# Kernel optimization log

Measured on AMD Instinct MI355X. Metric: run time of the kernel, lower is better.

Reference implementation:

```python
import jax, jax.numpy as jnp
import numpy as np

FACTOR = 5


def setup_inputs() -> dict:
    key = jax.random.key(0)
    k1, k2, k3 = jax.random.split(key, 3)
    B, L, H, E = 8, 3072, 8, 64
    return {
        "queries": jax.random.normal(k1, (B, L, H, E), dtype=jnp.float32),
        "keys": jax.random.normal(k2, (B, L, H, E), dtype=jnp.float32),
        "values": jax.random.normal(k3, (B, L, H, E), dtype=jnp.float32),
        "attn_mask": jnp.zeros((1,), dtype=jnp.int32),  # unused, matches torch signature
    }


def _autocorrelation(queries, keys, values):
    B, L, H, E = queries.shape
    # L == S here, so keys/values are used as-is (torch path: values[:, :L])
    qp = jnp.transpose(queries, (0, 2, 3, 1))  # [B,H,E,L]
    kp = jnp.transpose(keys, (0, 2, 3, 1))     # [B,H,E,L]
    vp = jnp.transpose(values, (0, 2, 3, 1))   # [B,H,D,L]

    # period-based dependencies via FFT cross-correlation
    q_fft = jnp.fft.rfft(qp, axis=-1)
    k_fft = jnp.fft.rfft(kp, axis=-1)
    corr = jnp.fft.irfft(q_fft * jnp.conj(k_fft), n=L, axis=-1)  # [B,H,E,L]

    # time-delay aggregation (training branch of the torch module)
    top_k = int(FACTOR * np.log(L))  # static (L known at trace time)
    mean_value = corr.mean(axis=1).mean(axis=1)            # [B,L]
    weights, index = jax.lax.top_k(mean_value, top_k)      # [B,K]
    tmp_corr = jax.nn.softmax(weights, axis=-1)            # [B,K]

    # torch uses only batch-0 shifts: roll(v, -index[0,i]) == gather (t + s) mod L
    shifts = index[0]                                      # [K]
    gather_idx = (jnp.arange(L)[None, :] + shifts[:, None]) % L  # [K,L]

    def step(acc, lag):
        idx_k, w_k = lag                    # idx_k: [L], w_k: [B]
        pattern = vp[..., idx_k]            # [B,H,D,L] rolled gather
        return acc + pattern * w_k[:, None, None, None], None

    agg, _ = jax.lax.scan(step, jnp.zeros_like(vp), (gather_idx, tmp_corr.T))
    return jnp.transpose(agg, (0, 3, 1, 2))  # [B,L,H,D]


def reference(queries, keys, values, attn_mask):
    return _autocorrelation(queries, keys, values)
```

## Files before the change

kernel.cpp:

```cpp
#include <hip/hip_runtime.h>
#include <math.h>

#define L_LEN  3072
#define CH512  512
#define TOPK   40
#define NBATCH 8
#define TWSZ   1088
#define SW(i)  ((i) + ((i) >> 5))
#define FFTSZ  3168
#define SW2(i) ((i) + ((i) >> 4))
#define FFTSZ2 3264

typedef __attribute__((ext_vector_type(2))) float f32x2;

__device__ __forceinline__ void fft3072(float* re, float* im,
                                        const float* Ctab, const float* Stab,
                                        int tid, float sgn)
{
    #pragma unroll
    for (int s = 0; s < 10; s += 2) {
        int q = 1 << s;
        #pragma unroll
        for (int ii = 0; ii < 3; ii++) {
            int ib  = tid + (ii << 8);
            int sub = ib >> 8;
            int t   = ib & 255;
            int pos = t & (q - 1);
            int base= t >> s;
            int i0  = (sub << 10) + (base << (s + 2)) + pos;
            int p0 = SW(i0), p1 = SW(i0 + q), p2 = SW(i0 + 2*q), p3 = SW(i0 + 3*q);
            int j2 = 3 * (pos << (8 - s));
            int ph = j2 + (j2 >> 4);
            float c2 = Ctab[ph], s2 = sgn * Stab[ph];
            float c1 = c2*c2 - s2*s2, s1 = 2.0f*c2*s2;
            float a0r = re[p0], a0i = im[p0];
            float a1r = re[p1], a1i = im[p1];
            float a2r = re[p2], a2i = im[p2];
            float a3r = re[p3], a3i = im[p3];
            float t1r = c1*a1r - s1*a1i, t1i = c1*a1i + s1*a1r;
            float u0r = a0r + t1r, u0i = a0i + t1i;
            float u1r = a0r - t1r, u1i = a0i - t1i;
            float t3r = c1*a3r - s1*a3i, t3i = c1*a3i + s1*a3r;
            float u2r = a2r + t3r, u2i = a2i + t3i;
            float u3r = a2r - t3r, u3i = a2i - t3i;
            float w2r = c2*u2r - s2*u2i, w2i = c2*u2i + s2*u2r;
            float w3r = c2*u3r - s2*u3i, w3i = c2*u3i + s2*u3r;
            float iw3r = -sgn * w3i, iw3i = sgn * w3r;
            re[p0] = u0r + w2r;  im[p0] = u0i + w2i;
            re[p2] = u0r - w2r;  im[p2] = u0i - w2i;
            re[p1] = u1r + iw3r; im[p1] = u1i + iw3i;
            re[p3] = u1r - iw3r; im[p3] = u1i - iw3i;
        }
        __syncthreads();
    }
    #pragma unroll
    for (int ii = 0; ii < 4; ii++) {
        int kk = tid + (ii << 8);
        int ph = kk + (kk >> 4);
        float c1 = Ctab[ph];
        float s1 = sgn * Stab[ph];
        float c2 = c1*c1 - s1*s1;
        float s2 = 2.0f*c1*s1;
        int pk0 = SW(kk), pk1 = SW(1024 + kk), pk2 = SW(2048 + kk);
        float y0r = re[pk0], y0i = im[pk0];
        float y1r = re[pk1], y1i = im[pk1];
        float y2r = re[pk2], y2i = im[pk2];
        float t1r = c1*y1r - s1*y1i, t1i = c1*y1i + s1*y1r;
        float t2r = c2*y2r - s2*y2i, t2i = c2*y2i + s2*y2r;
        float ur = t1r + t2r, ui = t1i + t2i;
        float vr = t1r - t2r, vi = t1i - t2i;
        float mr = y0r - 0.5f*ur, mi = y0i - 0.5f*ui;
        float s3 = sgn * 0.86602540378443864676f;
        re[pk0] = y0r + ur;      im[pk0] = y0i + ui;
        re[pk1] = mr - s3*vi;    im[pk1] = mi + s3*vr;
        re[pk2] = mr + s3*vi;    im[pk2] = mi - s3*vr;
    }
    __syncthreads();
}

__device__ __forceinline__ void fft3072p(f32x2* re, f32x2* im,
                                         const float* Ctab, const float* Stab,
                                         int tid, float sgn)
{
    #pragma unroll
    for (int s = 0; s < 10; s += 2) {
        int q = 1 << s;
        #pragma unroll
        for (int ii = 0; ii < 3; ii++) {
            int ib  = tid + (ii << 8);
            int sub = ib >> 8;
            int t   = ib & 255;
            int pos = t & (q - 1);
            int base= t >> s;
            int i0  = (sub << 10) + (base << (s + 2)) + pos;
            int p0 = SW2(i0), p1 = SW2(i0 + q), p2 = SW2(i0 + 2*q), p3 = SW2(i0 + 3*q);
            int j2 = 3 * (pos << (8 - s));
            int ph = j2 + (j2 >> 4);
            float c2 = Ctab[ph], s2 = sgn * Stab[ph];
            float c1 = c2*c2 - s2*s2, s1 = 2.0f*c2*s2;
            f32x2 a0r = re[p0], a0i = im[p0];
            f32x2 a1r = re[p1], a1i = im[p1];
            f32x2 a2r = re[p2], a2i = im[p2];
            f32x2 a3r = re[p3], a3i = im[p3];
            f32x2 t1r = c1*a1r - s1*a1i, t1i = c1*a1i + s1*a1r;
            f32x2 u0r = a0r + t1r, u0i = a0i + t1i;
            f32x2 u1r = a0r - t1r, u1i = a0i - t1i;
            f32x2 t3r = c1*a3r - s1*a3i, t3i = c1*a3i + s1*a3r;
            f32x2 u2r = a2r + t3r, u2i = a2i + t3i;
            f32x2 u3r = a2r - t3r, u3i = a2i - t3i;
            f32x2 w2r = c2*u2r - s2*u2i, w2i = c2*u2i + s2*u2r;
            f32x2 w3r = c2*u3r - s2*u3i, w3i = c2*u3i + s2*u3r;
            f32x2 iw3r = (-sgn) * w3i, iw3i = sgn * w3r;
            re[p0] = u0r + w2r;  im[p0] = u0i + w2i;
            re[p2] = u0r - w2r;  im[p2] = u0i - w2i;
            re[p1] = u1r + iw3r; im[p1] = u1i + iw3i;
            re[p3] = u1r - iw3r; im[p3] = u1i - iw3i;
        }
        __syncthreads();
    }
    #pragma unroll
    for (int ii = 0; ii < 4; ii++) {
        int kk = tid + (ii << 8);
        int ph = kk + (kk >> 4);
        float c1 = Ctab[ph];
        float s1 = sgn * Stab[ph];
        float c2 = c1*c1 - s1*s1;
        float s2 = 2.0f*c1*s1;
        int pk0 = SW2(kk), pk1 = SW2(1024 + kk), pk2 = SW2(2048 + kk);
        f32x2 y0r = re[pk0], y0i = im[pk0];
        f32x2 y1r = re[pk1], y1i = im[pk1];
        f32x2 y2r = re[pk2], y2i = im[pk2];
        f32x2 t1r = c1*y1r - s1*y1i, t1i = c1*y1i + s1*y1r;
        f32x2 t2r = c2*y2r - s2*y2i, t2i = c2*y2i + s2*y2r;
        f32x2 ur = t1r + t2r, ui = t1i + t2i;
        f32x2 vr = t1r - t2r, vi = t1i - t2i;
        f32x2 mr = y0r - 0.5f*ur, mi = y0i - 0.5f*ui;
        float s3 = sgn * 0.86602540378443864676f;
        re[pk0] = y0r + ur;      im[pk0] = y0i + ui;
        re[pk1] = mr - s3*vi;    im[pk1] = mi + s3*vr;
        re[pk2] = mr + s3*vi;    im[pk2] = mi - s3*vr;
    }
    __syncthreads();
}

__device__ __forceinline__ void fill_twiddles(float* Ctab, float* Stab, int tid)
{
    const float TWO_PI = 6.28318530717958647692f;
    for (int j = tid; j < 1024; j += 256) {
        float ang = TWO_PI * (float)j / 3072.0f;
        float c, s;
        __sincosf(ang, &s, &c);
        int ph = j + (j >> 4);
        Ctab[ph] = c; Stab[ph] = s;
    }
}

__global__ __launch_bounds__(256) void transpose_kernel(
    const float* __restrict__ q, const float* __restrict__ k,
    float* __restrict__ qT, float* __restrict__ kT)
{
    __shared__ float tile[64][65];
    int which = blockIdx.z & 1;
    int b     = blockIdx.z >> 1;
    int l0    = blockIdx.x << 6;
    int c0    = blockIdx.y << 6;
    int x4 = threadIdx.x & 15;
    int y  = threadIdx.x >> 4;
    const float* src = which ? k : q;
    float* dst       = which ? kT : qT;
    size_t in_base = (size_t)b * L_LEN * CH512;
    #pragma unroll
    for (int p = 0; p < 4; p++) {
        int r = y + (p << 4);
        float4 v = *(const float4*)(src + in_base + (size_t)(l0 + r) * CH512 + c0 + (x4 << 2));
        tile[r][(x4 << 2) + 0] = v.x;
        tile[r][(x4 << 2) + 1] = v.y;
        tile[r][(x4 << 2) + 2] = v.z;
        tile[r][(x4 << 2) + 3] = v.w;
    }
    __syncthreads();
    size_t out_base = (size_t)b * CH512 * L_LEN;
    #pragma unroll
    for (int p = 0; p < 4; p++) {
        int c = y + (p << 4);
        float4 w;
        w.x = tile[(x4 << 2) + 0][c];
        w.y = tile[(x4 << 2) + 1][c];
        w.z = tile[(x4 << 2) + 2][c];
        w.w = tile[(x4 << 2) + 3][c];
        *(float4*)(dst + out_base + (size_t)(c0 + c) * L_LEN + l0 + (x4 << 2)) = w;
    }
}

__global__ __launch_bounds__(256, 2) void corr_fft_kernel(
    const float* __restrict__ qT, const float* __restrict__ kT,
    float* __restrict__ S_re, float* __restrict__ S_im)
{
    __shared__ f32x2 re2[FFTSZ2], im2[FFTSZ2];
    __shared__ float Ctab[TWSZ], Stab[TWSZ];
    int blk = blockIdx.x;
    int b   = blk >> 7;
    int c0  = (blk & 127) << 2;
    int tid = threadIdx.x;

    fill_twiddles(Ctab, Stab, tid);

    float accR[12], accI[12];
    #pragma unroll
    for (int it = 0; it < 12; it++) { accR[it] = 0.0f; accI[it] = 0.0f; }

    for (int pp = 0; pp < 2; pp++) {
        int ca = c0 + (pp << 1);
        const float4* qa4 = (const float4*)(qT + ((size_t)b * CH512 + ca) * L_LEN);
        const float4* qb4 = (const float4*)(qT + ((size_t)b * CH512 + ca + 1) * L_LEN);
        const float4* ka4 = (const float4*)(kT + ((size_t)b * CH512 + ca) * L_LEN);
        const float4* kb4 = (const float4*)(kT + ((size_t)b * CH512 + ca + 1) * L_LEN);
        __syncthreads();
        #pragma unroll
        for (int it = 0; it < 3; it++) {
            int idx = tid + (it << 8);
            float4 xqa = qa4[idx], xqb = qb4[idx];
            float4 xka = ka4[idx], xkb = kb4[idx];
            #pragma unroll
            for (int j = 0; j < 4; j++) {
                int n = (idx << 2) + j;
                int m = n / 3;
                int r = n - 3 * m;
                int dst = SW2((r << 10) + (__brev((unsigned)m) >> 22));
                float qav = (j == 0) ? xqa.x : (j == 1) ? xqa.y : (j == 2) ? xqa.z : xqa.w;
                float qbv = (j == 0) ? xqb.x : (j == 1) ? xqb.y : (j == 2) ? xqb.z : xqb.w;
                float kav = (j == 0) ? xka.x : (j == 1) ? xka.y : (j == 2) ? xka.z : xka.w;
                float kbv = (j == 0) ? xkb.x : (j == 1) ? xkb.y : (j == 2) ? xkb.z : xkb.w;
                f32x2 vr = {qav, qbv};
                f32x2 vi = {kav, kbv};
                re2[dst] = vr;
                im2[dst] = vi;
            }
        }
        __syncthreads();
        fft3072p(re2, im2, Ctab, Stab, tid, -1.0f);
        #pragma unroll
        for (int it = 0; it < 12; it++) {
            int f = tid + (it << 8);
            int g = (f == 0) ? 0 : (L_LEN - f);
            int pf = SW2(f), pg = SW2(g);
            f32x2 ar = re2[pf], ai = im2[pf];
            f32x2 br = re2[pg], bi = -im2[pg];
            f32x2 ur = ar + br, ui = ai + bi;
            f32x2 vr = ar - br, vi = ai - bi;
            f32x2 pr = 0.25f * (ur * vi - ui * vr);
            f32x2 pi = 0.25f * (ur * vr + ui * vi);
            accR[it] += pr[0] + pr[1];
            accI[it] += pi[0] + pi[1];
        }
    }
    #pragma unroll
    for (int it = 0; it < 12; it++) {
        int f = tid + (it << 8);
        atomicAdd(&S_re[b * L_LEN + f], accR[it]);
        atomicAdd(&S_im[b * L_LEN + f], accI[it]);
    }
}

__global__ __launch_bounds__(256) void ifft_topk_kernel(
    const float* __restrict__ S_re, const float* __restrict__ S_im,
    float* __restrict__ wts, int* __restrict__ shifts)
{
    __shared__ float re[FFTSZ], im[FFTSZ];
    __shared__ float Ctab[TWSZ], Stab[TWSZ];
    __shared__ unsigned hist[256];
    __shared__ unsigned long long s_pref;
    __shared__ unsigned s_need;
    __shared__ unsigned s_cnt;
    __shared__ unsigned selk[TOPK];
    __shared__ unsigned selidx[TOPK];
    __shared__ float sv[TOPK];
    __shared__ int   si[TOPK];

    int b = blockIdx.x;
    int tid = threadIdx.x;
    fill_twiddles(Ctab, Stab, tid);
    #pragma unroll
    for (int it = 0; it < 12; it++) {
        int n = tid + (it << 8);
        int m = n / 3;
        int r = n - 3 * m;
        int dst = SW((r << 10) + (__brev((unsigned)m) >> 22));
        re[dst] = S_re[b * L_LEN + n];
        im[dst] = S_im[b * L_LEN + n];
    }
    __syncthreads();
    fft3072(re, im, Ctab, Stab, tid, 1.0f);

    unsigned* key = (unsigned*)im;
    const float scale = 1.0f / (3072.0f * 512.0f);
    #pragma unroll
    for (int it = 0; it < 12; it++) {
        int t = tid + (it << 8);
        float v = re[SW(t)] * scale;
        unsigned u = __float_as_uint(v);
        key[t] = (u & 0x80000000u) ? ~u : (u | 0x80000000u);
    }
    if (tid == 0) { s_pref = 0ULL; s_need = TOPK; s_cnt = 0u; }
    __syncthreads();

    #pragma unroll
    for (int p = 5; p >= 0; --p) {
        hist[tid] = 0u;
        __syncthreads();
        unsigned long long pref = s_pref;
        unsigned need = s_need;
        #pragma unroll
        for (int it = 0; it < 12; it++) {
            int t = tid + (it << 8);
            unsigned long long c = ((unsigned long long)key[t] << 12) | (unsigned)(4095 - t);
            if ((c >> ((p + 1) * 8)) == (pref >> ((p + 1) * 8)))
                atomicAdd(&hist[(unsigned)((c >> (p * 8)) & 0xFFu)], 1u);
        }
        __syncthreads();
        if (tid < 64) {
            int l = tid;
            unsigned s0 = hist[4*l] + hist[4*l+1] + hist[4*l+2] + hist[4*l+3];
            unsigned T = s0;
            #pragma unroll
            for (int off = 1; off < 64; off <<= 1) {
                unsigned o = __shfl_down(T, off);
                if (l + off < 64) T += o;
            }
            unsigned above = T - s0;
            if (T >= need && above < need) {
                unsigned acc = above;
                int bin = -1;
                #pragma unroll
                for (int j = 3; j >= 0; --j) {
                    unsigned h = hist[4*l + j];
                    if (bin < 0) {
                        if (acc + h >= need) bin = 4*l + j;
                        else acc += h;
                    }
                }
                s_pref = pref | ((unsigned long long)(unsigned)bin << (p * 8));
                s_need = need - acc;
            }
        }
        __syncthreads();
    }

    unsigned long long cstar = s_pref;
    #pragma unroll
    for (int it = 0; it < 12; it++) {
        int t = tid + (it << 8);
        unsigned long long c = ((unsigned long long)key[t] << 12) | (unsigned)(4095 - t);
        if (c >= cstar) {
            unsigned pos = atomicAdd(&s_cnt, 1u);
            if (pos < TOPK) { selk[pos] = key[t]; selidx[pos] = (unsigned)t; }
        }
    }
    __syncthreads();

    if (tid < TOPK) {
        unsigned mk = selk[tid], mi = selidx[tid];
        unsigned long long mc = ((unsigned long long)mk << 12) | (unsigned)(4095 - mi);
        int rank = 0;
        #pragma unroll
        for (int j = 0; j < TOPK; j++) {
            unsigned long long cj = ((unsigned long long)selk[j] << 12) | (unsigned)(4095 - selidx[j]);
            rank += (cj > mc) ? 1 : 0;
        }
        unsigned u = (mk & 0x80000000u) ? (mk ^ 0x80000000u) : ~mk;
        sv[rank] = __uint_as_float(u);
        si[rank] = (int)mi;
    }
    __syncthreads();

    if (tid == 0) {
        float mx = sv[0];
        float sum = 0.0f;
        float ex[TOPK];
        for (int kk = 0; kk < TOPK; kk++) { ex[kk] = __expf(sv[kk] - mx); sum += ex[kk]; }
        float inv = 1.0f / sum;
        for (int kk = 0; kk < TOPK; kk++) wts[b * TOPK + kk] = ex[kk] * inv;
        if (b == 0)
            for (int kk = 0; kk < TOPK; kk++) shifts[kk] = si[kk];
    }
}

__global__ __launch_bounds__(512) void agg_kernel(
    const float* __restrict__ v, const float* __restrict__ wts,
    const int* __restrict__ shifts, float* __restrict__ out)
{
    __shared__ float4 vcol[L_LEN];
    __shared__ float w[TOPK];
    __shared__ int   sh[TOPK];
    int pid = blockIdx.x;
    int idx = ((pid & 7) << 7) + (pid >> 3);
    int cg  = idx & 127;
    int b   = idx >> 7;
    int tid = threadIdx.x;
    int ch  = cg << 2;
    if (tid < TOPK) { w[tid] = wts[b * TOPK + tid]; sh[tid] = shifts[tid]; }
    size_t vbase = (size_t)b * L_LEN * CH512 + ch;
    #pragma unroll
    for (int it = 0; it < 6; it++) {
        int r = tid + (it << 9);
        vcol[r] = *(const float4*)(v + vbase + (size_t)r * CH512);
    }
    __syncthreads();
    float4 acc0 = make_float4(0.f,0.f,0.f,0.f);
    float4 acc1 = acc0, acc2 = acc0, acc3 = acc0, acc4 = acc0, acc5 = acc0;
    #pragma unroll 8
    for (int kk = 0; kk < TOPK; kk++) {
        float ww = w[kk];
        int s = sh[kk];
        int t0 = tid + s;            if (t0 >= L_LEN) t0 -= L_LEN;
        int t1 = tid + 512 + s;      if (t1 >= L_LEN) t1 -= L_LEN;
        int t2 = tid + 1024 + s;     if (t2 >= L_LEN) t2 -= L_LEN;
        int t3 = tid + 1536 + s;     if (t3 >= L_LEN) t3 -= L_LEN;
        int t4 = tid + 2048 + s;     if (t4 >= L_LEN) t4 -= L_LEN;
        int t5 = tid + 2560 + s;     if (t5 >= L_LEN) t5 -= L_LEN;
        float4 x0 = vcol[t0], x1 = vcol[t1], x2 = vcol[t2];
        float4 x3 = vcol[t3], x4 = vcol[t4], x5 = vcol[t5];
        acc0.x += x0.x*ww; acc0.y += x0.y*ww; acc0.z += x0.z*ww; acc0.w += x0.w*ww;
        acc1.x += x1.x*ww; acc1.y += x1.y*ww; acc1.z += x1.z*ww; acc1.w += x1.w*ww;
        acc2.x += x2.x*ww; acc2.y += x2.y*ww; acc2.z += x2.z*ww; acc2.w += x2.w*ww;
        acc3.x += x3.x*ww; acc3.y += x3.y*ww; acc3.z += x3.z*ww; acc3.w += x3.w*ww;
        acc4.x += x4.x*ww; acc4.y += x4.y*ww; acc4.z += x4.z*ww; acc4.w += x4.w*ww;
        acc5.x += x5.x*ww; acc5.y += x5.y*ww; acc5.z += x5.z*ww; acc5.w += x5.w*ww;
    }
    *(float4*)(out + vbase + (size_t)(tid         ) * CH512) = acc0;
    *(float4*)(out + vbase + (size_t)(tid + 512   ) * CH512) = acc1;
    *(float4*)(out + vbase + (size_t)(tid + 1024  ) * CH512) = acc2;
    *(float4*)(out + vbase + (size_t)(tid + 1536  ) * CH512) = acc3;
    *(float4*)(out + vbase + (size_t)(tid + 2048  ) * CH512) = acc4;
    *(float4*)(out + vbase + (size_t)(tid + 2560  ) * CH512) = acc5;
}

extern "C" void kernel_launch(void* const* d_in, const int* in_sizes, int n_in,
                              void* d_out, int out_size, void* d_ws, size_t ws_size,
                              hipStream_t stream)
{
    const float* q = (const float*)d_in[0];
    const float* k = (const float*)d_in[1];
    const float* v = (const float*)d_in[2];
    float* out = (float*)d_out;
    float* ws  = (float*)d_ws;

    const size_t TSZ = (size_t)NBATCH * CH512 * L_LEN;

    float* qT = out;
    float* kT = ws;
    float* S_re = ws + TSZ;
    float* S_im = S_re + NBATCH * L_LEN;
    float* wts  = S_im + NBATCH * L_LEN;
    int*   shifts = (int*)(wts + NBATCH * TOPK);

    hipMemsetAsync(S_re, 0, (size_t)2 * NBATCH * L_LEN * sizeof(float), stream);

    transpose_kernel<<<dim3(L_LEN / 64, CH512 / 64, NBATCH * 2), dim3(256), 0, stream>>>(
        q, k, qT, kT);
    corr_fft_kernel<<<dim3(1024), dim3(256), 0, stream>>>(qT, kT, S_re, S_im);
    ifft_topk_kernel<<<dim3(NBATCH), dim3(256), 0, stream>>>(S_re, S_im, wts, shifts);
    agg_kernel<<<dim3(NBATCH * (CH512 / 4)), dim3(512), 0, stream>>>(v, wts, shifts, out);
}
```

Before: 294.5 us.

## Fuse transpose into correlation FFT kernel and compute twiddles on the fly

Drops the separate transpose kernel. The FFT kernel now reads q and k directly in their [B,L,C] layout with strided float2 loads, so the transposed copies are never written to or read back from global memory. The twiddle tables in shared memory are replaced by __sincosf calls inside the FFT, which frees LDS and allows occupancy to rise to 3 blocks per CU. Blocks are also reordered to interleave batches. The strided 8-byte loads are less coalesced than the old float4 row reads, so memory efficiency may suffer, and recomputing twiddles adds ALU work.

```diff
diff --git a/kernel.cpp b/kernel.cpp
--- a/kernel.cpp
+++ b/kernel.cpp
@@ -78,10 +78,9 @@
     __syncthreads();
 }
 
-__device__ __forceinline__ void fft3072p(f32x2* re, f32x2* im,
-                                         const float* Ctab, const float* Stab,
-                                         int tid, float sgn)
-{
+__device__ __forceinline__ void fft3072p(f32x2* re, f32x2* im, int tid, float sgn)
+{
+    const float W = 6.28318530717958647692f / 3072.0f;
     #pragma unroll
     for (int s = 0; s < 10; s += 2) {
         int q = 1 << s;
@@ -95,8 +94,9 @@
             int i0  = (sub << 10) + (base << (s + 2)) + pos;
             int p0 = SW2(i0), p1 = SW2(i0 + q), p2 = SW2(i0 + 2*q), p3 = SW2(i0 + 3*q);
             int j2 = 3 * (pos << (8 - s));
-            int ph = j2 + (j2 >> 4);
-            float c2 = Ctab[ph], s2 = sgn * Stab[ph];
+            float c2, s2v;
+            __sincosf(W * (float)j2, &s2v, &c2);
+            float s2 = sgn * s2v;
             float c1 = c2*c2 - s2*s2, s1 = 2.0f*c2*s2;
             f32x2 a0r = re[p0], a0i = im[p0];
             f32x2 a1r = re[p1], a1i = im[p1];
@@ -121,9 +121,9 @@
     #pragma unroll
     for (int ii = 0; ii < 4; ii++) {
         int kk = tid + (ii << 8);
-        int ph = kk + (kk >> 4);
-        float c1 = Ctab[ph];
-        float s1 = sgn * Stab[ph];
+        float c1, s1v;
+        __sincosf(W * (float)kk, &s1v, &c1);
+        float s1 = sgn * s1v;
         float c2 = c1*c1 - s1*s1;
         float s2 = 2.0f*c1*s1;
         int pk0 = SW2(kk), pk1 = SW2(1024 + kk), pk2 = SW2(2048 + kk);
@@ -155,90 +155,41 @@
     }
 }
 
-__global__ __launch_bounds__(256) void transpose_kernel(
+__global__ __launch_bounds__(256, 3) void corr_fft_kernel(
     const float* __restrict__ q, const float* __restrict__ k,
-    float* __restrict__ qT, float* __restrict__ kT)
-{
-    __shared__ float tile[64][65];
-    int which = blockIdx.z & 1;
-    int b     = blockIdx.z >> 1;
-    int l0    = blockIdx.x << 6;
-    int c0    = blockIdx.y << 6;
-    int x4 = threadIdx.x & 15;
-    int y  = threadIdx.x >> 4;
-    const float* src = which ? k : q;
-    float* dst       = which ? kT : qT;
-    size_t in_base = (size_t)b * L_LEN * CH512;
-    #pragma unroll
-    for (int p = 0; p < 4; p++) {
-        int r = y + (p << 4);
-        float4 v = *(const float4*)(src + in_base + (size_t)(l0 + r) * CH512 + c0 + (x4 << 2));
-        tile[r][(x4 << 2) + 0] = v.x;
-        tile[r][(x4 << 2) + 1] = v.y;
-        tile[r][(x4 << 2) + 2] = v.z;
-        tile[r][(x4 << 2) + 3] = v.w;
-    }
-    __syncthreads();
-    size_t out_base = (size_t)b * CH512 * L_LEN;
-    #pragma unroll
-    for (int p = 0; p < 4; p++) {
-        int c = y + (p << 4);
-        float4 w;
-        w.x = tile[(x4 << 2) + 0][c];
-        w.y = tile[(x4 << 2) + 1][c];
-        w.z = tile[(x4 << 2) + 2][c];
-        w.w = tile[(x4 << 2) + 3][c];
-        *(float4*)(dst + out_base + (size_t)(c0 + c) * L_LEN + l0 + (x4 << 2)) = w;
-    }
-}
-
-__global__ __launch_bounds__(256, 2) void corr_fft_kernel(
-    const float* __restrict__ qT, const float* __restrict__ kT,
     float* __restrict__ S_re, float* __restrict__ S_im)
 {
     __shared__ f32x2 re2[FFTSZ2], im2[FFTSZ2];
-    __shared__ float Ctab[TWSZ], Stab[TWSZ];
-    int blk = blockIdx.x;
+    int pid = blockIdx.x;
+    int blk = ((pid & 7) << 7) + (pid >> 3);
     int b   = blk >> 7;
     int c0  = (blk & 127) << 2;
     int tid = threadIdx.x;
 
-    fill_twiddles(Ctab, Stab, tid);
-
     float accR[12], accI[12];
     #pragma unroll
     for (int it = 0; it < 12; it++) { accR[it] = 0.0f; accI[it] = 0.0f; }
 
     for (int pp = 0; pp < 2; pp++) {
         int ca = c0 + (pp << 1);
-        const float4* qa4 = (const float4*)(qT + ((size_t)b * CH512 + ca) * L_LEN);
-        const float4* qb4 = (const float4*)(qT + ((size_t)b * CH512 + ca + 1) * L_LEN);
-        const float4* ka4 = (const float4*)(kT + ((size_t)b * CH512 + ca) * L_LEN);
-        const float4* kb4 = (const float4*)(kT + ((size_t)b * CH512 + ca + 1) * L_LEN);
-        __syncthreads();
-        #pragma unroll
-        for (int it = 0; it < 3; it++) {
-            int idx = tid + (it << 8);
-            float4 xqa = qa4[idx], xqb = qb4[idx];
-            float4 xka = ka4[idx], xkb = kb4[idx];
-            #pragma unroll
-            for (int j = 0; j < 4; j++) {
-                int n = (idx << 2) + j;
-                int m = n / 3;
-                int r = n - 3 * m;
-                int dst = SW2((r << 10) + (__brev((unsigned)m) >> 22));
-                float qav = (j == 0) ? xqa.x : (j == 1) ? xqa.y : (j == 2) ? xqa.z : xqa.w;
-                float qbv = (j == 0) ? xqb.x : (j == 1) ? xqb.y : (j == 2) ? xqb.z : xqb.w;
-                float kav = (j == 0) ? xka.x : (j == 1) ? xka.y : (j == 2) ? xka.z : xka.w;
-                float kbv = (j == 0) ? xkb.x : (j == 1) ? xkb.y : (j == 2) ? xkb.z : xkb.w;
-                f32x2 vr = {qav, qbv};
-                f32x2 vi = {kav, kbv};
-                re2[dst] = vr;
-                im2[dst] = vi;
-            }
-        }
-        __syncthreads();
-        fft3072p(re2, im2, Ctab, Stab, tid, -1.0f);
+        const float* qb_ = q + (size_t)b * L_LEN * CH512 + ca;
+        const float* kb_ = k + (size_t)b * L_LEN * CH512 + ca;
+        __syncthreads();
+        #pragma unroll
+        for (int it = 0; it < 12; it++) {
+            int t = tid + (it << 8);
+            float2 xq = *(const float2*)(qb_ + (size_t)t * CH512);
+            float2 xk = *(const float2*)(kb_ + (size_t)t * CH512);
+            int m = t / 3;
+            int r = t - 3 * m;
+            int dst = SW2((r << 10) + (__brev((unsigned)m) >> 22));
+            f32x2 vr = {xq.x, xq.y};
+            f32x2 vi = {xk.x, xk.y};
+            re2[dst] = vr;
+            im2[dst] = vi;
+        }
+        __syncthreads();
+        fft3072p(re2, im2, tid, -1.0f);
         #pragma unroll
         for (int it = 0; it < 12; it++) {
             int f = tid + (it << 8);
@@ -445,20 +396,14 @@
     float* out = (float*)d_out;
     float* ws  = (float*)d_ws;
 
-    const size_t TSZ = (size_t)NBATCH * CH512 * L_LEN;
-
-    float* qT = out;
-    float* kT = ws;
-    float* S_re = ws + TSZ;
+    float* S_re = ws;
     float* S_im = S_re + NBATCH * L_LEN;
     float* wts  = S_im + NBATCH * L_LEN;
     int*   shifts = (int*)(wts + NBATCH * TOPK);
 
     hipMemsetAsync(S_re, 0, (size_t)2 * NBATCH * L_LEN * sizeof(float), stream);
 
-    transpose_kernel<<<dim3(L_LEN / 64, CH512 / 64, NBATCH * 2), dim3(256), 0, stream>>>(
-        q, k, qT, kT);
-    corr_fft_kernel<<<dim3(1024), dim3(256), 0, stream>>>(qT, kT, S_re, S_im);
+    corr_fft_kernel<<<dim3(1024), dim3(256), 0, stream>>>(q, k, S_re, S_im);
     ifft_topk_kernel<<<dim3(NBATCH), dim3(256), 0, stream>>>(S_re, S_im, wts, shifts);
     agg_kernel<<<dim3(NBATCH * (CH512 / 4)), dim3(512), 0, stream>>>(v, wts, shifts, out);
 }
```

New measurement: 332.1 us. 12.8% more time.
